# Kernel optimization log

Hardware: AMD Instinct MI355X
Metric: run time of the kernel (lower is better)

The kernel has to match this reference:

```python
import jax, jax.numpy as jnp
import numpy as np

N = 50000


def gcn_conv(x, edge_index, W, b):
    # PyG GCNConv: h = XW; add self-loops; sym-normalized scatter-add; + bias
    n = x.shape[0]
    h = x @ W  # [N, out]
    loop = jnp.arange(n)
    src = jnp.concatenate([edge_index[0], loop])
    dst = jnp.concatenate([edge_index[1], loop])
    deg = jax.ops.segment_sum(jnp.ones_like(dst, dtype=h.dtype), dst, num_segments=n)
    dinv = jax.lax.rsqrt(jnp.maximum(deg, 1.0))  # deg >= 1 after self-loops
    norm = dinv[src] * dinv[dst]  # [E+N]
    msg = h[src] * norm[:, None]  # [E+N, out]
    return jax.ops.segment_sum(msg, dst, num_segments=n) + b


def setup_inputs() -> dict:
    key = jax.random.key(0)
    ks = jax.random.split(key, 20)
    E = 1600000
    inp = {
        "metadata_a": jax.random.normal(ks[0], (N, 512), jnp.float32),
        "metadata_b": jax.random.normal(ks[1], (N, 512), jnp.float32),
        "x_a": jax.random.normal(ks[2], (N, 256), jnp.float32),
        "x_b": jax.random.normal(ks[3], (N, 256), jnp.float32),
        "edge_index_a": jax.random.randint(ks[4], (2, E), 0, N, dtype=jnp.int64),
        "edge_index_b": jax.random.randint(ks[5], (2, E), 0, N, dtype=jnp.int64),
        # parameters (fan-in scaled)
        "fc1_W": jax.random.normal(ks[6], (512, 128), jnp.float32) / np.sqrt(512),
        "fc1_b": jnp.zeros((128,), jnp.float32),
        "fc2_W": jax.random.normal(ks[7], (128, 128), jnp.float32) / np.sqrt(128),
        "fc2_b": jnp.zeros((128,), jnp.float32),
        "gcn1_W": jax.random.normal(ks[8], (256, 128), jnp.float32) / np.sqrt(256),
        "gcn1_b": jnp.zeros((128,), jnp.float32),
        "gcn2_W": jax.random.normal(ks[9], (128, 128), jnp.float32) / np.sqrt(128),
        "gcn2_b": jnp.zeros((128,), jnp.float32),
        "fcc_W": jax.random.normal(ks[10], (512, 128), jnp.float32) / np.sqrt(512),
        "fcc_b": jnp.zeros((128,), jnp.float32),
        "out_W": jax.random.normal(ks[11], (128, 1), jnp.float32) / np.sqrt(128),
        "out_b": jnp.zeros((1,), jnp.float32),
    }
    return inp


def reference(metadata_a, metadata_b, x_a, x_b, edge_index_a, edge_index_b,
              fc1_W, fc1_b, fc2_W, fc2_b, gcn1_W, gcn1_b, gcn2_W, gcn2_b,
              fcc_W, fcc_b, out_W, out_b):
    def mlp(m):
        m = jax.nn.relu(m @ fc1_W + fc1_b)
        return jax.nn.relu(m @ fc2_W + fc2_b)

    def gcn_branch(x, ei):
        x = jax.nn.relu(gcn_conv(x, ei, gcn1_W, gcn1_b))
        return jax.nn.relu(gcn_conv(x, ei, gcn2_W, gcn2_b))

    ma = mlp(metadata_a)
    mb = mlp(metadata_b)
    ga = gcn_branch(x_a, edge_index_a)
    gb = gcn_branch(x_b, edge_index_b)
    combined = jnp.concatenate([ma, mb, ga, gb], axis=1)  # [N, 512]
    combined = jax.nn.relu(combined @ fcc_W + fcc_b)
    return jax.nn.sigmoid(combined @ out_W + out_b)  # [N, 1]
```

## Files before the change

### kernel.cpp

```cpp
#include <hip/hip_runtime.h>
#include <math.h>


typedef __attribute__((ext_vector_type(8))) short bf16x8;
typedef __attribute__((ext_vector_type(4))) float f32x4;

static __device__ __forceinline__ unsigned short f2bf(float f) {
  unsigned u = __float_as_uint(f);
  unsigned r = u + 0x7fffu + ((u >> 16) & 1u);
  return (unsigned short)(r >> 16);
}
static __device__ __forceinline__ float bf2f(unsigned short h) {
  return __uint_as_float(((unsigned)h) << 16);
}
static __device__ __forceinline__ float bflo(unsigned m) { return __uint_as_float(m << 16); }
static __device__ __forceinline__ float bfhi(unsigned m) { return __uint_as_float(m & 0xffff0000u); }

#define GM 128

__launch_bounds__(256)
__global__ void gemm_mfma(const void* __restrict__ Av, int lda, int a_fp32,
                          const unsigned short* __restrict__ Wt,
                          const float* __restrict__ bias,
                          const float* __restrict__ rowscale,
                          unsigned short* __restrict__ Cb,
                          float* __restrict__ Cf,
                          int ldc, int col_off,
                          int M, int K, int do_relu) {
  const int tid = threadIdx.x;
  const int wave = tid >> 6;
  const int lane = tid & 63;
  const int quad = lane >> 4;
  const int lr = lane & 15;
  const int m0 = blockIdx.x * GM + wave * 32;

  f32x4 acc[2][8];
#pragma unroll
  for (int r = 0; r < 2; r++)
#pragma unroll
    for (int c = 0; c < 8; c++) acc[r][c] = (f32x4){0.f, 0.f, 0.f, 0.f};

  int arow0 = m0 + lr;        if (arow0 > M - 1) arow0 = M - 1;
  int arow1 = m0 + 16 + lr;   if (arow1 > M - 1) arow1 = M - 1;

  const int KT = K >> 5;
  const bf16x8* Bf = (const bf16x8*)Wt;
  for (int kt = 0; kt < KT; kt++) {
    const int kq = kt * 32 + quad * 8;
    bf16x8 a[2];
    if (a_fp32) {
      const float* a0 = (const float*)Av + (size_t)arow0 * lda + kq;
      const float* a1 = (const float*)Av + (size_t)arow1 * lda + kq;
      float4 l0 = *(const float4*)a0, h0 = *(const float4*)(a0 + 4);
      float4 l1 = *(const float4*)a1, h1 = *(const float4*)(a1 + 4);
      a[0][0] = (short)f2bf(l0.x); a[0][1] = (short)f2bf(l0.y);
      a[0][2] = (short)f2bf(l0.z); a[0][3] = (short)f2bf(l0.w);
      a[0][4] = (short)f2bf(h0.x); a[0][5] = (short)f2bf(h0.y);
      a[0][6] = (short)f2bf(h0.z); a[0][7] = (short)f2bf(h0.w);
      a[1][0] = (short)f2bf(l1.x); a[1][1] = (short)f2bf(l1.y);
      a[1][2] = (short)f2bf(l1.z); a[1][3] = (short)f2bf(l1.w);
      a[1][4] = (short)f2bf(h1.x); a[1][5] = (short)f2bf(h1.y);
      a[1][6] = (short)f2bf(h1.z); a[1][7] = (short)f2bf(h1.w);
    } else {
      a[0] = *(const bf16x8*)((const unsigned short*)Av + (size_t)arow0 * lda + kq);
      a[1] = *(const bf16x8*)((const unsigned short*)Av + (size_t)arow1 * lda + kq);
    }
    const bf16x8* Bk = Bf + (size_t)kt * 512 + lane;
#pragma unroll
    for (int c = 0; c < 8; c++) {
      bf16x8 b = Bk[c * 64];
      acc[0][c] = __builtin_amdgcn_mfma_f32_16x16x32_bf16(a[0], b, acc[0][c], 0, 0, 0);
      acc[1][c] = __builtin_amdgcn_mfma_f32_16x16x32_bf16(a[1], b, acc[1][c], 0, 0, 0);
    }
  }

#pragma unroll
  for (int r = 0; r < 2; r++) {
    const int rbase = m0 + r * 16 + quad * 4;
    float rs[4];
#pragma unroll
    for (int i = 0; i < 4; i++) {
      int row = rbase + i;
      rs[i] = (rowscale && row < M) ? rowscale[row] : 1.0f;
    }
#pragma unroll
    for (int c = 0; c < 8; c++) {
      const int col = col_off + c * 16 + lr;
      const float bi = bias ? bias[c * 16 + lr] : 0.f;
#pragma unroll
      for (int i = 0; i < 4; i++) {
        int row = rbase + i;
        if (row < M) {
          float v = acc[r][c][i] * rs[i] + bi;
          if (do_relu) v = fmaxf(v, 0.f);
          if (Cb) Cb[(size_t)row * ldc + col] = f2bf(v);
          else    Cf[(size_t)row * ldc + col] = v;
        }
      }
    }
  }
}

__global__ void prep_w(const float* __restrict__ fc1, const float* __restrict__ fc2,
                       const float* __restrict__ g1, const float* __restrict__ g2,
                       const float* __restrict__ fcc, unsigned short* __restrict__ wt) {
  int t = blockIdx.x * 256 + threadIdx.x;
  const float* src[5] = {fc1, fc2, g1, g2, fcc};
  const int Ks[5] = {512, 128, 256, 128, 512};
  int off = 0;
#pragma unroll
  for (int w = 0; w < 5; w++) {
    int K = Ks[w];
    int ngroups = K * 16;
    if (t < ngroups) {
      int lane = t & 63;
      int c = (t >> 6) & 7;
      int kt = t >> 9;
      int quad = lane >> 4, lr = lane & 15;
      int n = c * 16 + lr;
      unsigned short* dst = wt + off + (size_t)t * 8;
      const float* s = src[w];
#pragma unroll
      for (int j = 0; j < 8; j++) {
        int k = kt * 32 + quad * 8 + j;
        dst[j] = f2bf(s[k * 128 + n]);
      }
    }
    off += K * 128;
  }
}

__launch_bounds__(256)
__global__ void bucket_hist(const int* __restrict__ eiA, const int* __restrict__ eiB,
                            int E, int T, int NB, int* __restrict__ bucket_cnt) {
  __shared__ int hist[128];
  const int g = blockIdx.x >= T;
  const int tile = blockIdx.x - g * T;
  const int* ei = g ? eiB : eiA;
  const int tid = threadIdx.x;
  for (int i = tid; i < NB; i += 256) hist[i] = 0;
  __syncthreads();
  const int base = tile * 4096;
#pragma unroll
  for (int j = 0; j < 16; j++) {
    int li = base + j * 256 + tid;
    if (li < E) atomicAdd(&hist[ei[E + li] >> 9], 1);
  }
  __syncthreads();
  for (int i = tid; i < NB; i += 256)
    if (hist[i]) atomicAdd(&bucket_cnt[g * NB + i], hist[i]);
}

__launch_bounds__(256)
__global__ void scan_buckets(const int* __restrict__ bucket_cnt, int E, int N, int NB,
                             int* __restrict__ bbase, int* __restrict__ gcur,
                             int* __restrict__ rpA, int* __restrict__ rpB) {
  __shared__ int sc[256];
  const int tid = threadIdx.x;
  if (tid < 2 * NB) sc[tid] = bucket_cnt[tid];
  __syncthreads();
  if (tid == 0) {
    for (int g = 0; g < 2; g++) {
      int acc = 0;
      for (int b = 0; b < NB; b++) {
        bbase[g * (NB + 1) + b] = acc;
        gcur[g * NB + b] = g * E + acc;
        acc += sc[g * NB + b];
      }
      bbase[g * (NB + 1) + NB] = acc;
    }
    rpA[N] = E;
    rpB[N] = E;
  }
}

__launch_bounds__(256)
__global__ void bucket_scatter(const int* __restrict__ eiA, const int* __restrict__ eiB,
                               int E, int T, int NB, int* __restrict__ gcur,
                               unsigned* __restrict__ records) {
  __shared__ unsigned staging[4096];
  __shared__ int hist[129];
  __shared__ int offs[129];
  __shared__ int gbase[128];
  __shared__ int sm[128];
  const int g = blockIdx.x >= T;
  const int tile = blockIdx.x - g * T;
  const int* ei = g ? eiB : eiA;
  const int tid = threadIdx.x;
  for (int i = tid; i <= NB; i += 256) hist[i] = 0;
  __syncthreads();
  const int base = tile * 4096;
  int myb[16], myp[16];
  unsigned myrec[16];
#pragma unroll
  for (int j = 0; j < 16; j++) {
    int li = base + j * 256 + tid;
    int b = NB;
    unsigned rec = 0;
    if (li < E) {
      int s = ei[li], d = ei[E + li];
      b = d >> 9;
      rec = (unsigned)s | ((unsigned)d << 16);
    }
    myb[j] = b; myrec[j] = rec;
    myp[j] = atomicAdd(&hist[b], 1);
  }
  __syncthreads();
  if (tid < 128) sm[tid] = (tid <= NB) ? hist[tid] : 0;
  __syncthreads();
  for (int d = 1; d < 128; d <<= 1) {
    int v = 0;
    if (tid < 128) { v = sm[tid]; if (tid >= d) v += sm[tid - d]; }
    __syncthreads();
    if (tid < 128) sm[tid] = v;
    __syncthreads();
  }
  if (tid < 128) offs[tid] = sm[tid] - ((tid <= NB) ? hist[tid] : 0);
  __syncthreads();
#pragma unroll
  for (int j = 0; j < 16; j++)
    if (myb[j] < NB) staging[offs[myb[j]] + myp[j]] = myrec[j];
  if (tid < NB && hist[tid] > 0) gbase[tid] = atomicAdd(&gcur[g * NB + tid], hist[tid]);
  __syncthreads();
  const int total = offs[NB];
  for (int i = tid; i < total; i += 256) {
    unsigned rec = staging[i];
    int b = (int)(rec >> 16) >> 9;
    records[gbase[b] + (i - offs[b])] = rec;
  }
}

__launch_bounds__(256)
__global__ void csr_build(const unsigned* __restrict__ records, const int* __restrict__ bbase,
                          int E, int N, int NB,
                          int* __restrict__ rpA, int* __restrict__ rpB,
                          float* __restrict__ dinv,
                          unsigned short* __restrict__ csrA, unsigned short* __restrict__ csrB) {
  __shared__ int ncnt[512];
  __shared__ int excl[512];
  __shared__ int sm[256];
  const int g = blockIdx.x >= NB;
  const int b = blockIdx.x - g * NB;
  const int tid = threadIdx.x;
  const int base = bbase[g * (NB + 1) + b];
  const int cnt  = bbase[g * (NB + 1) + b + 1] - base;
  const int node0 = b << 9;
  const int nb = min(512, N - node0);
  const unsigned* rec = records + (size_t)g * E + base;
  int* rp = g ? rpB : rpA;
  unsigned short* csr = g ? csrB : csrA;

  for (int i = tid; i < 512; i += 256) ncnt[i] = 0;
  __syncthreads();
  for (int i = tid; i < cnt; i += 256)
    atomicAdd(&ncnt[(rec[i] >> 16) & 511], 1);
  __syncthreads();
  int a0 = ncnt[2 * tid], a1 = ncnt[2 * tid + 1];
  int ps = a0 + a1;
  sm[tid] = ps;
  __syncthreads();
  for (int d = 1; d < 256; d <<= 1) {
    int v = sm[tid];
    if (tid >= d) v += sm[tid - d];
    __syncthreads();
    sm[tid] = v;
    __syncthreads();
  }
  int e0 = sm[tid] - ps;
  excl[2 * tid] = e0;
  excl[2 * tid + 1] = e0 + a0;
  __syncthreads();
  for (int i = tid; i < nb; i += 256) {
    rp[node0 + i] = base + excl[i];
    dinv[g * N + node0 + i] = rsqrtf((float)(ncnt[i] + 1));
  }
  __syncthreads();
  for (int i = tid; i < 512; i += 256) ncnt[i] = excl[i];
  __syncthreads();
  for (int i = tid; i < cnt; i += 256) {
    unsigned r = rec[i];
    int p = atomicAdd(&ncnt[(r >> 16) & 511], 1);
    csr[base + p] = (unsigned short)(r & 0xffffu);
  }
}

#define ACC8(m)                                        \
  acc[0] += bflo((m).x); acc[1] += bfhi((m).x);        \
  acc[2] += bflo((m).y); acc[3] += bfhi((m).y);        \
  acc[4] += bflo((m).z); acc[5] += bfhi((m).z);        \
  acc[6] += bflo((m).w); acc[7] += bfhi((m).w);

__launch_bounds__(256)
__global__ void gather4(const unsigned short* __restrict__ hsA,
                        const unsigned short* __restrict__ hsB,
                        const unsigned short* __restrict__ csrA,
                        const unsigned short* __restrict__ csrB,
                        const int* __restrict__ rpA, const int* __restrict__ rpB,
                        const float* __restrict__ dinv,
                        const float* __restrict__ bias,
                        unsigned short* __restrict__ outA, unsigned short* __restrict__ outB,
                        int ldA, int coA, int ldB, int coB, int N) {
  int widx = (blockIdx.x * 256 + threadIdx.x) >> 6;
  if (widx >= 2 * N) return;
  int g = widx >= N;
  int v = g ? widx - N : widx;
  const unsigned short* hs = g ? hsB : hsA;
  const unsigned short* csr = g ? csrB : csrA;
  const int* rp = g ? rpB : rpA;
  unsigned short* out = g ? outB : outA;
  const int ldc = g ? ldB : ldA;
  const int co = g ? coB : coA;
  const int lane = threadIdx.x & 63;
  const int grp = lane >> 4;
  const int u = lane & 15;

  float acc[8];
#pragma unroll
  for (int j = 0; j < 8; j++) acc[j] = 0.f;

  int e = rp[v];
  const int end = rp[v + 1];
  for (; e + 8 <= end; e += 8) {
    int s0 = csr[e + grp];
    int s1 = csr[e + 4 + grp];
    uint4 m0 = *(const uint4*)(hs + (size_t)s0 * 128 + u * 8);
    uint4 m1 = *(const uint4*)(hs + (size_t)s1 * 128 + u * 8);
    ACC8(m0);
    ACC8(m1);
  }
  if (e + 4 <= end) {
    int s0 = csr[e + grp];
    uint4 m0 = *(const uint4*)(hs + (size_t)s0 * 128 + u * 8);
    ACC8(m0);
    e += 4;
  }
  int r = end - e;
  if (r > 0) {
    int s0 = csr[e + (grp < r ? grp : r - 1)];
    uint4 m = *(const uint4*)(hs + (size_t)s0 * 128 + u * 8);
    float msk = (grp < r) ? 1.f : 0.f;
    acc[0] = fmaf(msk, bflo(m.x), acc[0]); acc[1] = fmaf(msk, bfhi(m.x), acc[1]);
    acc[2] = fmaf(msk, bflo(m.y), acc[2]); acc[3] = fmaf(msk, bfhi(m.y), acc[3]);
    acc[4] = fmaf(msk, bflo(m.z), acc[4]); acc[5] = fmaf(msk, bfhi(m.z), acc[5]);
    acc[6] = fmaf(msk, bflo(m.w), acc[6]); acc[7] = fmaf(msk, bfhi(m.w), acc[7]);
  }

#pragma unroll
  for (int j = 0; j < 8; j++) {
    acc[j] += __shfl_down(acc[j], 32, 64);
    acc[j] += __shfl_down(acc[j], 16, 64);
  }
  if (grp == 0) {
    uint4 sm = *(const uint4*)(hs + (size_t)v * 128 + u * 8);
    ACC8(sm);
    float dv = dinv[g * N + v];
    float4 b0 = *(const float4*)(bias + u * 8);
    float4 b1 = *(const float4*)(bias + u * 8 + 4);
    float o0 = fmaxf(acc[0] * dv + b0.x, 0.f), o1 = fmaxf(acc[1] * dv + b0.y, 0.f);
    float o2 = fmaxf(acc[2] * dv + b0.z, 0.f), o3 = fmaxf(acc[3] * dv + b0.w, 0.f);
    float o4 = fmaxf(acc[4] * dv + b1.x, 0.f), o5 = fmaxf(acc[5] * dv + b1.y, 0.f);
    float o6 = fmaxf(acc[6] * dv + b1.z, 0.f), o7 = fmaxf(acc[7] * dv + b1.w, 0.f);
    uint4 P;
    P.x = (unsigned)f2bf(o0) | ((unsigned)f2bf(o1) << 16);
    P.y = (unsigned)f2bf(o2) | ((unsigned)f2bf(o3) << 16);
    P.z = (unsigned)f2bf(o4) | ((unsigned)f2bf(o5) << 16);
    P.w = (unsigned)f2bf(o6) | ((unsigned)f2bf(o7) << 16);
    *(uint4*)(out + (size_t)v * ldc + co + u * 8) = P;
  }
}

__launch_bounds__(256)
__global__ void final_out(const float* __restrict__ f, const float* __restrict__ outW,
                          const float* __restrict__ outb, float* __restrict__ y, int n) {
  int gw = (blockIdx.x * 256 + threadIdx.x) >> 6;
  int lane = threadIdx.x & 63;
  if (gw >= n) return;
  const float2* fr = (const float2*)(f + (size_t)gw * 128);
  const float2* w2 = (const float2*)outW;
  float2 a = fr[lane], b = w2[lane];
  float p = a.x * b.x + a.y * b.y;
#pragma unroll
  for (int off = 32; off > 0; off >>= 1) p += __shfl_down(p, off, 64);
  if (lane == 0) y[gw] = 1.f / (1.f + expf(-(p + outb[0])));
}

extern "C" void kernel_launch(void* const* d_in, const int* in_sizes, int n_in,
                              void* d_out, int out_size, void* d_ws, size_t ws_size,
                              hipStream_t stream) {
  const float* meta_a = (const float*)d_in[0];
  const float* meta_b = (const float*)d_in[1];
  const float* x_a    = (const float*)d_in[2];
  const float* x_b    = (const float*)d_in[3];
  const int*   ei_a   = (const int*)d_in[4];
  const int*   ei_b   = (const int*)d_in[5];
  const float* fc1_W = (const float*)d_in[6];
  const float* fc1_b = (const float*)d_in[7];
  const float* fc2_W = (const float*)d_in[8];
  const float* fc2_b = (const float*)d_in[9];
  const float* gcn1_W = (const float*)d_in[10];
  const float* gcn1_b = (const float*)d_in[11];
  const float* gcn2_W = (const float*)d_in[12];
  const float* gcn2_b = (const float*)d_in[13];
  const float* fcc_W = (const float*)d_in[14];
  const float* fcc_b = (const float*)d_in[15];
  const float* out_W = (const float*)d_in[16];
  const float* out_b = (const float*)d_in[17];
  float* y = (float*)d_out;

  const int N = in_sizes[0] / 512;
  const int E = in_sizes[4] / 2;
  const int NB = (N + 511) >> 9;
  const int T = (E + 4095) / 4096;

  char* p = (char*)d_ws;
  auto alloc = [&](size_t bytes) { char* r = p; p += (bytes + 255) & ~255ull; return r; };
  unsigned short* combined = (unsigned short*)alloc((size_t)N * 512 * 2);
  unsigned short* t0 = (unsigned short*)alloc((size_t)N * 128 * 2);
  unsigned short* t1 = (unsigned short*)alloc((size_t)N * 128 * 2);
  unsigned short* t2 = (unsigned short*)alloc((size_t)N * 128 * 2);
  unsigned short* t3 = (unsigned short*)alloc((size_t)N * 128 * 2);
  unsigned short* wt = (unsigned short*)alloc(196608 * 2);
  float* dinv = (float*)alloc((size_t)2 * N * 4);
  int* rpA = (int*)alloc((size_t)(N + 1) * 4);
  int* rpB = (int*)alloc((size_t)(N + 1) * 4);
  int* bucket_cnt = (int*)alloc((size_t)2 * NB * 4);
  int* bbase = (int*)alloc((size_t)2 * (NB + 1) * 4);
  int* gcur = (int*)alloc((size_t)2 * NB * 4);
  size_t rec_bytes = ((size_t)2 * E * 4 + 255) & ~255ull;
  size_t csr_bytes = ((size_t)E * 2 + 255) & ~255ull;
  size_t big_bytes = rec_bytes + 2 * csr_bytes;
  size_t fcc_bytes = (size_t)N * 128 * 4;
  char* big = alloc(big_bytes > fcc_bytes ? big_bytes : fcc_bytes);
  unsigned* records = (unsigned*)big;
  unsigned short* csrA = (unsigned short*)(big + rec_bytes);
  unsigned short* csrB = (unsigned short*)(big + rec_bytes + csr_bytes);
  float* fccout = (float*)big;

  unsigned short* wt_fc1 = wt;
  unsigned short* wt_fc2 = wt + 65536;
  unsigned short* wt_g1  = wt + 81920;
  unsigned short* wt_g2  = wt + 114688;
  unsigned short* wt_fcc = wt + 131072;

  const int gemm_grid = (N + GM - 1) / GM;

  prep_w<<<32, 256, 0, stream>>>(fc1_W, fc2_W, gcn1_W, gcn2_W, fcc_W, wt);
  hipMemsetAsync(bucket_cnt, 0, (size_t)2 * NB * 4, stream);
  bucket_hist<<<2 * T, 256, 0, stream>>>(ei_a, ei_b, E, T, NB, bucket_cnt);
  scan_buckets<<<1, 256, 0, stream>>>(bucket_cnt, E, N, NB, bbase, gcur, rpA, rpB);
  bucket_scatter<<<2 * T, 256, 0, stream>>>(ei_a, ei_b, E, T, NB, gcur, records);
  csr_build<<<2 * NB, 256, 0, stream>>>(records, bbase, E, N, NB, rpA, rpB, dinv, csrA, csrB);

  gemm_mfma<<<gemm_grid, 256, 0, stream>>>(meta_a, 512, 1, wt_fc1, fc1_b, nullptr, t0, nullptr, 128, 0, N, 512, 1);
  gemm_mfma<<<gemm_grid, 256, 0, stream>>>(t0, 128, 0, wt_fc2, fc2_b, nullptr, combined, nullptr, 512, 0, N, 128, 1);
  gemm_mfma<<<gemm_grid, 256, 0, stream>>>(meta_b, 512, 1, wt_fc1, fc1_b, nullptr, t0, nullptr, 128, 0, N, 512, 1);
  gemm_mfma<<<gemm_grid, 256, 0, stream>>>(t0, 128, 0, wt_fc2, fc2_b, nullptr, combined, nullptr, 512, 128, N, 128, 1);

  gemm_mfma<<<gemm_grid, 256, 0, stream>>>(x_a, 256, 1, wt_g1, nullptr, dinv,     t0, nullptr, 128, 0, N, 256, 0);
  gemm_mfma<<<gemm_grid, 256, 0, stream>>>(x_b, 256, 1, wt_g1, nullptr, dinv + N, t1, nullptr, 128, 0, N, 256, 0);
  gather4<<<(2 * N + 3) / 4, 256, 0, stream>>>(t0, t1, csrA, csrB, rpA, rpB, dinv, gcn1_b,
                                               t2, t3, 128, 0, 128, 0, N);
  gemm_mfma<<<gemm_grid, 256, 0, stream>>>(t2, 128, 0, wt_g2, nullptr, dinv,     t0, nullptr, 128, 0, N, 128, 0);
  gemm_mfma<<<gemm_grid, 256, 0, stream>>>(t3, 128, 0, wt_g2, nullptr, dinv + N, t1, nullptr, 128, 0, N, 128, 0);
  gather4<<<(2 * N + 3) / 4, 256, 0, stream>>>(t0, t1, csrA, csrB, rpA, rpB, dinv, gcn2_b,
                                               combined, combined, 512, 256, 512, 384, N);

  gemm_mfma<<<gemm_grid, 256, 0, stream>>>(combined, 512, 0, wt_fcc, fcc_b, nullptr, nullptr, fccout, 128, 0, N, 512, 1);
  final_out<<<(N + 3) / 4, 256, 0, stream>>>(fccout, out_W, out_b, y, N);
}
```

Before: 843.7 us.

## Batch paired branch GEMMs into single launches and unroll neighbor gather 16-wide

The GEMM kernel now takes two input and two output pointers and splits its rows at Mh. This lets the a and b branches of the MLP layers and both GCN linear layers run in one launch over 2N rows, cutting GEMM launches from 9 to 5. Each launch also gets a grid twice as large, which should fill the GPU better. The gather kernel processes 16 edges per iteration with two independent accumulators, so more row loads are in flight per wave. The trade-off is more register pressure and some per-row branching in the GEMM to pick a pointer and column offset.

```diff
diff --git a/kernel.cpp b/kernel.cpp
--- a/kernel.cpp
+++ b/kernel.cpp
@@ -19,14 +19,15 @@
 #define GM 128
 
 __launch_bounds__(256)
-__global__ void gemm_mfma(const void* __restrict__ Av, int lda, int a_fp32,
+__global__ void gemm_mfma(const void* __restrict__ Av, const void* __restrict__ Av2,
+                          int lda, int a_fp32,
                           const unsigned short* __restrict__ Wt,
                           const float* __restrict__ bias,
                           const float* __restrict__ rowscale,
-                          unsigned short* __restrict__ Cb,
-                          float* __restrict__ Cf,
-                          int ldc, int col_off,
-                          int M, int K, int do_relu) {
+                          unsigned short* __restrict__ Cb, unsigned short* __restrict__ Cb2,
+                          float* __restrict__ Cf, float* __restrict__ Cf2,
+                          int ldc, int co, int co2,
+                          int Mh, int M, int K, int do_relu) {
   const int tid = threadIdx.x;
   const int wave = tid >> 6;
   const int lane = tid & 63;
@@ -40,8 +41,13 @@
 #pragma unroll
     for (int c = 0; c < 8; c++) acc[r][c] = (f32x4){0.f, 0.f, 0.f, 0.f};
 
-  int arow0 = m0 + lr;        if (arow0 > M - 1) arow0 = M - 1;
-  int arow1 = m0 + 16 + lr;   if (arow1 > M - 1) arow1 = M - 1;
+  int rg0 = m0 + lr;        if (rg0 > M - 1) rg0 = M - 1;
+  int rg1 = m0 + 16 + lr;   if (rg1 > M - 1) rg1 = M - 1;
+  const int h0 = rg0 >= Mh, h1 = rg1 >= Mh;
+  const int rl0 = rg0 - (h0 ? Mh : 0);
+  const int rl1 = rg1 - (h1 ? Mh : 0);
+  const char* base0 = (const char*)(h0 ? Av2 : Av);
+  const char* base1 = (const char*)(h1 ? Av2 : Av);
 
   const int KT = K >> 5;
   const bf16x8* Bf = (const bf16x8*)Wt;
@@ -49,21 +55,21 @@
     const int kq = kt * 32 + quad * 8;
     bf16x8 a[2];
     if (a_fp32) {
-      const float* a0 = (const float*)Av + (size_t)arow0 * lda + kq;
-      const float* a1 = (const float*)Av + (size_t)arow1 * lda + kq;
-      float4 l0 = *(const float4*)a0, h0 = *(const float4*)(a0 + 4);
-      float4 l1 = *(const float4*)a1, h1 = *(const float4*)(a1 + 4);
+      const float* a0 = (const float*)base0 + (size_t)rl0 * lda + kq;
+      const float* a1 = (const float*)base1 + (size_t)rl1 * lda + kq;
+      float4 l0 = *(const float4*)a0, hh0 = *(const float4*)(a0 + 4);
+      float4 l1 = *(const float4*)a1, hh1 = *(const float4*)(a1 + 4);
       a[0][0] = (short)f2bf(l0.x); a[0][1] = (short)f2bf(l0.y);
       a[0][2] = (short)f2bf(l0.z); a[0][3] = (short)f2bf(l0.w);
-      a[0][4] = (short)f2bf(h0.x); a[0][5] = (short)f2bf(h0.y);
-      a[0][6] = (short)f2bf(h0.z); a[0][7] = (short)f2bf(h0.w);
+      a[0][4] = (short)f2bf(hh0.x); a[0][5] = (short)f2bf(hh0.y);
+      a[0][6] = (short)f2bf(hh0.z); a[0][7] = (short)f2bf(hh0.w);
       a[1][0] = (short)f2bf(l1.x); a[1][1] = (short)f2bf(l1.y);
       a[1][2] = (short)f2bf(l1.z); a[1][3] = (short)f2bf(l1.w);
-      a[1][4] = (short)f2bf(h1.x); a[1][5] = (short)f2bf(h1.y);
-      a[1][6] = (short)f2bf(h1.z); a[1][7] = (short)f2bf(h1.w);
+      a[1][4] = (short)f2bf(hh1.x); a[1][5] = (short)f2bf(hh1.y);
+      a[1][6] = (short)f2bf(hh1.z); a[1][7] = (short)f2bf(hh1.w);
     } else {
-      a[0] = *(const bf16x8*)((const unsigned short*)Av + (size_t)arow0 * lda + kq);
-      a[1] = *(const bf16x8*)((const unsigned short*)Av + (size_t)arow1 * lda + kq);
+      a[0] = *(const bf16x8*)((const unsigned short*)base0 + (size_t)rl0 * lda + kq);
+      a[1] = *(const bf16x8*)((const unsigned short*)base1 + (size_t)rl1 * lda + kq);
     }
     const bf16x8* Bk = Bf + (size_t)kt * 512 + lane;
 #pragma unroll
@@ -85,16 +91,23 @@
     }
 #pragma unroll
     for (int c = 0; c < 8; c++) {
-      const int col = col_off + c * 16 + lr;
-      const float bi = bias ? bias[c * 16 + lr] : 0.f;
+      const int nc = c * 16 + lr;
+      const float bi = bias ? bias[nc] : 0.f;
 #pragma unroll
       for (int i = 0; i < 4; i++) {
         int row = rbase + i;
         if (row < M) {
+          int h = row >= Mh;
+          int rl = row - (h ? Mh : 0);
           float v = acc[r][c][i] * rs[i] + bi;
           if (do_relu) v = fmaxf(v, 0.f);
-          if (Cb) Cb[(size_t)row * ldc + col] = f2bf(v);
-          else    Cf[(size_t)row * ldc + col] = v;
+          if (Cb) {
+            unsigned short* C = h ? Cb2 : Cb;
+            C[(size_t)rl * ldc + (h ? co2 : co) + nc] = f2bf(v);
+          } else {
+            float* C = h ? Cf2 : Cf;
+            C[(size_t)rl * ldc + (h ? co2 : co) + nc] = v;
+          }
         }
       }
     }
@@ -284,22 +297,24 @@
   }
 }
 
-#define ACC8(m)                                        \
-  acc[0] += bflo((m).x); acc[1] += bfhi((m).x);        \
-  acc[2] += bflo((m).y); acc[3] += bfhi((m).y);        \
-  acc[4] += bflo((m).z); acc[5] += bfhi((m).z);        \
-  acc[6] += bflo((m).w); acc[7] += bfhi((m).w);
-
-__launch_bounds__(256)
-__global__ void gather4(const unsigned short* __restrict__ hsA,
-                        const unsigned short* __restrict__ hsB,
-                        const unsigned short* __restrict__ csrA,
-                        const unsigned short* __restrict__ csrB,
-                        const int* __restrict__ rpA, const int* __restrict__ rpB,
-                        const float* __restrict__ dinv,
-                        const float* __restrict__ bias,
-                        unsigned short* __restrict__ outA, unsigned short* __restrict__ outB,
-                        int ldA, int coA, int ldB, int coB, int N) {
+struct f2x4 { float2 a, b, c, d; };
+static __device__ __forceinline__ void acc2(f2x4& A, const uint4& m) {
+  A.a.x += bflo(m.x); A.a.y += bfhi(m.x);
+  A.b.x += bflo(m.y); A.b.y += bfhi(m.y);
+  A.c.x += bflo(m.z); A.c.y += bfhi(m.z);
+  A.d.x += bflo(m.w); A.d.y += bfhi(m.w);
+}
+
+__launch_bounds__(256)
+__global__ void gather16(const unsigned short* __restrict__ hsA,
+                         const unsigned short* __restrict__ hsB,
+                         const unsigned short* __restrict__ csrA,
+                         const unsigned short* __restrict__ csrB,
+                         const int* __restrict__ rpA, const int* __restrict__ rpB,
+                         const float* __restrict__ dinv,
+                         const float* __restrict__ bias,
+                         unsigned short* __restrict__ outA, unsigned short* __restrict__ outB,
+                         int ldA, int coA, int ldB, int coB, int N) {
   int widx = (blockIdx.x * 256 + threadIdx.x) >> 6;
   if (widx >= 2 * N) return;
   int g = widx >= N;
@@ -313,46 +328,53 @@
   const int lane = threadIdx.x & 63;
   const int grp = lane >> 4;
   const int u = lane & 15;
-
-  float acc[8];
-#pragma unroll
-  for (int j = 0; j < 8; j++) acc[j] = 0.f;
+  const unsigned short* rowb = hs + u * 8;
+
+  f2x4 A0 = {{0,0},{0,0},{0,0},{0,0}};
+  f2x4 A1 = {{0,0},{0,0},{0,0},{0,0}};
 
   int e = rp[v];
   const int end = rp[v + 1];
-  for (; e + 8 <= end; e += 8) {
+  for (; e + 16 <= end; e += 16) {
     int s0 = csr[e + grp];
     int s1 = csr[e + 4 + grp];
-    uint4 m0 = *(const uint4*)(hs + (size_t)s0 * 128 + u * 8);
-    uint4 m1 = *(const uint4*)(hs + (size_t)s1 * 128 + u * 8);
-    ACC8(m0);
-    ACC8(m1);
-  }
-  if (e + 4 <= end) {
+    int s2 = csr[e + 8 + grp];
+    int s3 = csr[e + 12 + grp];
+    uint4 m0 = *(const uint4*)(rowb + (size_t)s0 * 128);
+    uint4 m1 = *(const uint4*)(rowb + (size_t)s1 * 128);
+    uint4 m2 = *(const uint4*)(rowb + (size_t)s2 * 128);
+    uint4 m3 = *(const uint4*)(rowb + (size_t)s3 * 128);
+    acc2(A0, m0); acc2(A1, m1); acc2(A0, m2); acc2(A1, m3);
+  }
+  for (; e + 4 <= end; e += 4) {
     int s0 = csr[e + grp];
-    uint4 m0 = *(const uint4*)(hs + (size_t)s0 * 128 + u * 8);
-    ACC8(m0);
-    e += 4;
+    uint4 m0 = *(const uint4*)(rowb + (size_t)s0 * 128);
+    acc2(A0, m0);
   }
   int r = end - e;
   if (r > 0) {
     int s0 = csr[e + (grp < r ? grp : r - 1)];
-    uint4 m = *(const uint4*)(hs + (size_t)s0 * 128 + u * 8);
+    uint4 m = *(const uint4*)(rowb + (size_t)s0 * 128);
     float msk = (grp < r) ? 1.f : 0.f;
-    acc[0] = fmaf(msk, bflo(m.x), acc[0]); acc[1] = fmaf(msk, bfhi(m.x), acc[1]);
-    acc[2] = fmaf(msk, bflo(m.y), acc[2]); acc[3] = fmaf(msk, bfhi(m.y), acc[3]);
-    acc[4] = fmaf(msk, bflo(m.z), acc[4]); acc[5] = fmaf(msk, bfhi(m.z), acc[5]);
-    acc[6] = fmaf(msk, bflo(m.w), acc[6]); acc[7] = fmaf(msk, bfhi(m.w), acc[7]);
-  }
-
+    A1.a.x = fmaf(msk, bflo(m.x), A1.a.x); A1.a.y = fmaf(msk, bfhi(m.x), A1.a.y);
+    A1.b.x = fmaf(msk, bflo(m.y), A1.b.x); A1.b.y = fmaf(msk, bfhi(m.y), A1.b.y);
+    A1.c.x = fmaf(msk, bflo(m.z), A1.c.x); A1.c.y = fmaf(msk, bfhi(m.z), A1.c.y);
+    A1.d.x = fmaf(msk, bflo(m.w), A1.d.x); A1.d.y = fmaf(msk, bfhi(m.w), A1.d.y);
+  }
+
+  float acc[8] = {A0.a.x + A1.a.x, A0.a.y + A1.a.y, A0.b.x + A1.b.x, A0.b.y + A1.b.y,
+                  A0.c.x + A1.c.x, A0.c.y + A1.c.y, A0.d.x + A1.d.x, A0.d.y + A1.d.y};
 #pragma unroll
   for (int j = 0; j < 8; j++) {
     acc[j] += __shfl_down(acc[j], 32, 64);
     acc[j] += __shfl_down(acc[j], 16, 64);
   }
   if (grp == 0) {
-    uint4 sm = *(const uint4*)(hs + (size_t)v * 128 + u * 8);
-    ACC8(sm);
+    uint4 smv = *(const uint4*)(rowb + (size_t)v * 128);
+    acc[0] += bflo(smv.x); acc[1] += bfhi(smv.x);
+    acc[2] += bflo(smv.y); acc[3] += bfhi(smv.y);
+    acc[4] += bflo(smv.z); acc[5] += bfhi(smv.z);
+    acc[6] += bflo(smv.w); acc[7] += bfhi(smv.w);
     float dv = dinv[g * N + v];
     float4 b0 = *(const float4*)(bias + u * 8);
     float4 b1 = *(const float4*)(bias + u * 8 + 4);
@@ -442,7 +464,8 @@
   unsigned short* wt_g2  = wt + 114688;
   unsigned short* wt_fcc = wt + 131072;
 
-  const int gemm_grid = (N + GM - 1) / GM;
+  const int grid1 = (N + GM - 1) / GM;
+  const int grid2 = (2 * N + GM - 1) / GM;
 
   prep_w<<<32, 256, 0, stream>>>(fc1_W, fc2_W, gcn1_W, gcn2_W, fcc_W, wt);
   hipMemsetAsync(bucket_cnt, 0, (size_t)2 * NB * 4, stream);
@@ -451,20 +474,21 @@
   bucket_scatter<<<2 * T, 256, 0, stream>>>(ei_a, ei_b, E, T, NB, gcur, records);
   csr_build<<<2 * NB, 256, 0, stream>>>(records, bbase, E, N, NB, rpA, rpB, dinv, csrA, csrB);
 
-  gemm_mfma<<<gemm_grid, 256, 0, stream>>>(meta_a, 512, 1, wt_fc1, fc1_b, nullptr, t0, nullptr, 128, 0, N, 512, 1);
-  gemm_mfma<<<gemm_grid, 256, 0, stream>>>(t0, 128, 0, wt_fc2, fc2_b, nullptr, combined, nullptr, 512, 0, N, 128, 1);
-  gemm_mfma<<<gemm_grid, 256, 0, stream>>>(meta_b, 512, 1, wt_fc1, fc1_b, nullptr, t0, nullptr, 128, 0, N, 512, 1);
-  gemm_mfma<<<gemm_grid, 256, 0, stream>>>(t0, 128, 0, wt_fc2, fc2_b, nullptr, combined, nullptr, 512, 128, N, 128, 1);
-
-  gemm_mfma<<<gemm_grid, 256, 0, stream>>>(x_a, 256, 1, wt_g1, nullptr, dinv,     t0, nullptr, 128, 0, N, 256, 0);
-  gemm_mfma<<<gemm_grid, 256, 0, stream>>>(x_b, 256, 1, wt_g1, nullptr, dinv + N, t1, nullptr, 128, 0, N, 256, 0);
-  gather4<<<(2 * N + 3) / 4, 256, 0, stream>>>(t0, t1, csrA, csrB, rpA, rpB, dinv, gcn1_b,
-                                               t2, t3, 128, 0, 128, 0, N);
-  gemm_mfma<<<gemm_grid, 256, 0, stream>>>(t2, 128, 0, wt_g2, nullptr, dinv,     t0, nullptr, 128, 0, N, 128, 0);
-  gemm_mfma<<<gemm_grid, 256, 0, stream>>>(t3, 128, 0, wt_g2, nullptr, dinv + N, t1, nullptr, 128, 0, N, 128, 0);
-  gather4<<<(2 * N + 3) / 4, 256, 0, stream>>>(t0, t1, csrA, csrB, rpA, rpB, dinv, gcn2_b,
-                                               combined, combined, 512, 256, 512, 384, N);
-
-  gemm_mfma<<<gemm_grid, 256, 0, stream>>>(combined, 512, 0, wt_fcc, fcc_b, nullptr, nullptr, fccout, 128, 0, N, 512, 1);
+  gemm_mfma<<<grid2, 256, 0, stream>>>(meta_a, meta_b, 512, 1, wt_fc1, fc1_b, nullptr,
+                                       t0, t1, nullptr, nullptr, 128, 0, 0, N, 2 * N, 512, 1);
+  gemm_mfma<<<grid2, 256, 0, stream>>>(t0, t1, 128, 0, wt_fc2, fc2_b, nullptr,
+                                       combined, combined, nullptr, nullptr, 512, 0, 128, N, 2 * N, 128, 1);
+
+  gemm_mfma<<<grid2, 256, 0, stream>>>(x_a, x_b, 256, 1, wt_g1, nullptr, dinv,
+                                       t0, t1, nullptr, nullptr, 128, 0, 0, N, 2 * N, 256, 0);
+  gather16<<<(2 * N + 3) / 4, 256, 0, stream>>>(t0, t1, csrA, csrB, rpA, rpB, dinv, gcn1_b,
+                                                t2, t3, 128, 0, 128, 0, N);
+  gemm_mfma<<<grid2, 256, 0, stream>>>(t2, t3, 128, 0, wt_g2, nullptr, dinv,
+                                       t0, t1, nullptr, nullptr, 128, 0, 0, N, 2 * N, 128, 0);
+  gather16<<<(2 * N + 3) / 4, 256, 0, stream>>>(t0, t1, csrA, csrB, rpA, rpB, dinv, gcn2_b,
+                                                combined, combined, 512, 256, 512, 384, N);
+
+  gemm_mfma<<<grid1, 256, 0, stream>>>(combined, combined, 512, 0, wt_fcc, fcc_b, nullptr,
+                                       nullptr, nullptr, fccout, fccout, 128, 0, 0, N, N, 512, 1);
   final_out<<<(N + 3) / 4, 256, 0, stream>>>(fccout, out_W, out_b, y, N);
 }
```

Result: slower. 862.2 us (+2.2%).
